# Kernel tuning notes

Hardware: AMD Instinct MI355X
Metric: run time of the kernel (lower is better)

Reference implementation:

```python
import jax, jax.numpy as jnp
import numpy as np

EPS = 1e-5
NH = 4          # num_heads
DH = 128        # head_dim
ALPHA = 1.0 / float(np.sqrt(DH))


def _ln(x, w, b):
    m = x.mean(-1, keepdims=True)
    v = x.var(-1, keepdims=True)
    return (x - m) * jax.lax.rsqrt(v + EPS) * w + b


def setup_inputs() -> dict:
    key = jax.random.key(0)
    ks = jax.random.split(key, 8)
    D = 512                 # hidden_size
    U = 4 * NH * DH         # uvqk linear out = 2048
    B, S, H = 32, 256, 2048  # batch, new tokens/seq, history len/seq
    NT = B * S              # 8192 flattened jagged tokens
    layer_input = jax.random.normal(ks[0], (NT, D), dtype=jnp.float32)
    hist_k = jax.random.normal(ks[1], (B, H, NH, DH), dtype=jnp.float32) * 0.1
    hist_v = jax.random.normal(ks[2], (B, H, NH, DH), dtype=jnp.float32) * 0.1
    # torch init: uniform(-0.5, 0.5); scaled down for numerical sanity
    W_uvqk = (jax.random.uniform(ks[3], (D, U), dtype=jnp.float32) - 0.5) * 0.1
    b_uvqk = (jax.random.uniform(ks[4], (U,), dtype=jnp.float32) - 0.5) * 0.1
    ln_in_w = jnp.ones((D,), jnp.float32)
    ln_in_b = jnp.zeros((D,), jnp.float32)
    ln_out_w = jnp.ones((NH * DH,), jnp.float32)
    ln_out_b = jnp.zeros((NH * DH,), jnp.float32)
    W_proj = jax.random.normal(ks[5], (NH * DH, D), dtype=jnp.float32) * 0.05
    return {
        "layer_input": layer_input, "hist_k": hist_k, "hist_v": hist_v,
        "ln_in_w": ln_in_w, "ln_in_b": ln_in_b,
        "W_uvqk": W_uvqk, "b_uvqk": b_uvqk,
        "ln_out_w": ln_out_w, "ln_out_b": ln_out_b, "W_proj": W_proj,
    }


def reference(layer_input, hist_k, hist_v, ln_in_w, ln_in_b,
              W_uvqk, b_uvqk, ln_out_w, ln_out_b, W_proj):
    B, H, nh, dh = hist_k.shape
    NT, D = layer_input.shape
    S = NT // B
    dspl = nh * dh
    # ln -> linear+bias -> silu (fused u,v,q,k projection)
    x = _ln(layer_input, ln_in_w, ln_in_b)
    uvqk = jax.nn.silu(x @ W_uvqk + b_uvqk)
    u, v, q, k = jnp.split(uvqk, 4, axis=-1)   # order: user, value, query, key
    q = q.reshape(B, S, nh, dh)
    k = k.reshape(B, S, nh, dh)
    v = v.reshape(B, S, nh, dh)
    # paged KV-cache append == concat new k,v after history
    K = jnp.concatenate([hist_k, k], axis=1)   # [B, T, nh, dh], T = H+S
    V = jnp.concatenate([hist_v, v], axis=1)
    T = H + S
    # HSTU varlen attention: silu(alpha * q k^T) with causal delta-q mask,
    # query i sits at global position H+i and may attend to kv pos <= H+i
    scores = jnp.einsum('bsnd,btnd->bnst', q, K) * ALPHA
    mask = jnp.arange(T)[None, :] <= (H + jnp.arange(S))[:, None]  # [S, T]
    p = jnp.where(mask[None, None], jax.nn.silu(scores), 0.0)
    attn = jnp.einsum('bnst,btnd->bsnd', p, V).reshape(NT, dspl)
    # gated output LN, projection, residual
    parallel = u * _ln(attn, ln_out_w, ln_out_b)
    return parallel @ W_proj + layer_input
```

## Files before the change

kernel.cpp:

```cpp
#include <hip/hip_runtime.h>
#include <hip/hip_bf16.h>


typedef __attribute__((ext_vector_type(8))) short v8s;
typedef __attribute__((ext_vector_type(4))) float v4f;
typedef __attribute__((ext_vector_type(4))) unsigned short v4us;
typedef __attribute__((ext_vector_type(4))) unsigned int v4u;

#define D_HID 512
#define U_DIM 2048
#define NHEAD 4
#define DHEAD 128
#define BATCH 32
#define SEQ   256
#define HIST  2048
#define NTOK  8192
#define ALPHA_ 0.08838834764831845f
#define EPS_   1e-5f

__device__ __forceinline__ unsigned short f2bf(float f) {
  unsigned int u = __float_as_uint(f);
  u += 0x7FFFu + ((u >> 16) & 1u);
  return (unsigned short)(u >> 16);
}
__device__ __forceinline__ float bf2f(unsigned short s) {
  return __uint_as_float(((unsigned int)s) << 16);
}
__device__ __forceinline__ float siluf(float x) {
  return x / (1.0f + __expf(-x));
}
__device__ __forceinline__ unsigned int cvtpk(float lo, float hi) {
  __hip_bfloat162 h = __float22bfloat162_rn(make_float2(lo, hi));
  union { __hip_bfloat162 h; unsigned int u; } cv; cv.h = h;
  return cv.u;
}

__global__ __launch_bounds__(256) void ln_in_kernel(
    const float* __restrict__ x, const float* __restrict__ w,
    const float* __restrict__ b, unsigned short* __restrict__ out)
{
  int wid = threadIdx.x >> 6, lane = threadIdx.x & 63;
  int row = blockIdx.x * 4 + wid;
  const float* xr = x + (size_t)row * D_HID + lane * 8;
  float4 a0 = *(const float4*)xr;
  float4 a1 = *(const float4*)(xr + 4);
  float v[8] = {a0.x, a0.y, a0.z, a0.w, a1.x, a1.y, a1.z, a1.w};
  float s = 0.f, s2 = 0.f;
#pragma unroll
  for (int j = 0; j < 8; ++j) { s += v[j]; s2 += v[j] * v[j]; }
#pragma unroll
  for (int m = 1; m < 64; m <<= 1) { s += __shfl_xor(s, m, 64); s2 += __shfl_xor(s2, m, 64); }
  float mean = s * (1.f / D_HID);
  float var  = s2 * (1.f / D_HID) - mean * mean;
  float rstd = rsqrtf(var + EPS_);
  const float* wp = w + lane * 8; const float* bp = b + lane * 8;
  float4 w0 = *(const float4*)wp, w1 = *(const float4*)(wp + 4);
  float4 b0 = *(const float4*)bp, b1 = *(const float4*)(bp + 4);
  float wv[8] = {w0.x, w0.y, w0.z, w0.w, w1.x, w1.y, w1.z, w1.w};
  float bv[8] = {b0.x, b0.y, b0.z, b0.w, b1.x, b1.y, b1.z, b1.w};
  v8s o;
#pragma unroll
  for (int j = 0; j < 8; ++j) o[j] = (short)f2bf((v[j] - mean) * rstd * wv[j] + bv[j]);
  *(v8s*)(out + (size_t)row * D_HID + lane * 8) = o;
}

__global__ __launch_bounds__(256) void gated_ln_kernel(
    const float* __restrict__ attn0, const float* __restrict__ attn1,
    const unsigned short* __restrict__ uvqk,
    const float* __restrict__ w, const float* __restrict__ b,
    unsigned short* __restrict__ par)
{
  int wid = threadIdx.x >> 6, lane = threadIdx.x & 63;
  int row = blockIdx.x * 4 + wid;
  size_t off = (size_t)row * D_HID + lane * 8;
  float4 x0 = *(const float4*)(attn0 + off), x1 = *(const float4*)(attn0 + off + 4);
  float4 y0 = *(const float4*)(attn1 + off), y1 = *(const float4*)(attn1 + off + 4);
  float v[8] = {x0.x + y0.x, x0.y + y0.y, x0.z + y0.z, x0.w + y0.w,
                x1.x + y1.x, x1.y + y1.y, x1.z + y1.z, x1.w + y1.w};
  float s = 0.f, s2 = 0.f;
#pragma unroll
  for (int j = 0; j < 8; ++j) { s += v[j]; s2 += v[j] * v[j]; }
#pragma unroll
  for (int m = 1; m < 64; m <<= 1) { s += __shfl_xor(s, m, 64); s2 += __shfl_xor(s2, m, 64); }
  float mean = s * (1.f / D_HID);
  float var  = s2 * (1.f / D_HID) - mean * mean;
  float rstd = rsqrtf(var + EPS_);
  const float* wp = w + lane * 8; const float* bp = b + lane * 8;
  float4 w0 = *(const float4*)wp, w1 = *(const float4*)(wp + 4);
  float4 b0 = *(const float4*)bp, b1 = *(const float4*)(bp + 4);
  float wv[8] = {w0.x, w0.y, w0.z, w0.w, w1.x, w1.y, w1.z, w1.w};
  float bv[8] = {b0.x, b0.y, b0.z, b0.w, b1.x, b1.y, b1.z, b1.w};
  v8s uv = *(const v8s*)(uvqk + (size_t)row * U_DIM + lane * 8);
  v8s o;
#pragma unroll
  for (int j = 0; j < 8; ++j) {
    float u = bf2f((unsigned short)uv[j]);
    o[j] = (short)f2bf(u * ((v[j] - mean) * rstd * wv[j] + bv[j]));
  }
  *(v8s*)(par + (size_t)row * D_HID + lane * 8) = o;
}

__global__ __launch_bounds__(256) void transpose_w_kernel(
    const float* __restrict__ in, unsigned short* __restrict__ out, int R, int C)
{
  __shared__ float tile[32][33];
  int c0 = blockIdx.x * 32, r0 = blockIdx.y * 32;
  int tr = threadIdx.x >> 3;
  int tc = (threadIdx.x & 7) * 4;
  float4 vv = *(const float4*)(in + (size_t)(r0 + tr) * C + c0 + tc);
  tile[tr][tc + 0] = vv.x; tile[tr][tc + 1] = vv.y;
  tile[tr][tc + 2] = vv.z; tile[tr][tc + 3] = vv.w;
  __syncthreads();
  v4us o;
#pragma unroll
  for (int j = 0; j < 4; ++j) o[j] = f2bf(tile[tc + j][tr]);
  *(v4us*)(out + (size_t)(c0 + tr) * R + r0 + tc) = o;
}

template <int EPI>
__global__ __launch_bounds__(256) void gemm_kernel(
    const unsigned short* __restrict__ A, const unsigned short* __restrict__ Bt,
    int K, int N,
    const float* __restrict__ bias, const float* __restrict__ resid,
    unsigned short* __restrict__ outb, float* __restrict__ outf)
{
  __shared__ unsigned short Al[128 * 40];
  __shared__ unsigned short Bl[128 * 40];
  int m0 = blockIdx.x * 128, n0 = blockIdx.y * 128;
  int tid = threadIdx.x, lane = tid & 63, wid = tid >> 6;
  int wr = wid >> 1, wc = wid & 1;
  int lr = lane & 15, lg = lane >> 4;

  v4f acc[4][4];
#pragma unroll
  for (int i = 0; i < 4; ++i)
#pragma unroll
    for (int j = 0; j < 4; ++j) acc[i][j] = (v4f){0.f, 0.f, 0.f, 0.f};

  int srow = tid >> 1;
  int sc   = (tid & 1) * 16;
  const unsigned short* ga = A  + (size_t)(m0 + srow) * K + sc;
  const unsigned short* gb = Bt + (size_t)(n0 + srow) * K + sc;

  for (int k0 = 0; k0 < K; k0 += 32) {
    v8s a0 = *(const v8s*)(ga + k0);
    v8s a1 = *(const v8s*)(ga + k0 + 8);
    v8s b0 = *(const v8s*)(gb + k0);
    v8s b1 = *(const v8s*)(gb + k0 + 8);
    *(v8s*)&Al[srow * 40 + sc]     = a0;
    *(v8s*)&Al[srow * 40 + sc + 8] = a1;
    *(v8s*)&Bl[srow * 40 + sc]     = b0;
    *(v8s*)&Bl[srow * 40 + sc + 8] = b1;
    __syncthreads();
    v8s af[4], bf[4];
#pragma unroll
    for (int mt = 0; mt < 4; ++mt) af[mt] = *(const v8s*)&Al[(wr * 64 + mt * 16 + lr) * 40 + lg * 8];
#pragma unroll
    for (int nt = 0; nt < 4; ++nt) bf[nt] = *(const v8s*)&Bl[(wc * 64 + nt * 16 + lr) * 40 + lg * 8];
#pragma unroll
    for (int mt = 0; mt < 4; ++mt)
#pragma unroll
      for (int nt = 0; nt < 4; ++nt)
        acc[mt][nt] = __builtin_amdgcn_mfma_f32_16x16x32_bf16(af[mt], bf[nt], acc[mt][nt], 0, 0, 0);
    __syncthreads();
  }

#pragma unroll
  for (int nt = 0; nt < 4; ++nt) {
    int col = n0 + wc * 64 + nt * 16 + lr;
    float bi = 0.f;
    if constexpr (EPI == 0) bi = bias[col];
#pragma unroll
    for (int mt = 0; mt < 4; ++mt) {
      int row0 = m0 + wr * 64 + mt * 16 + lg * 4;
#pragma unroll
      for (int r = 0; r < 4; ++r) {
        float xv = acc[mt][nt][r];
        if constexpr (EPI == 0) {
          float rv = siluf(xv + bi);
          if ((unsigned)(col - 2 * D_HID) < (unsigned)D_HID) rv *= ALPHA_;
          outb[(size_t)(row0 + r) * N + col] = f2bf(rv);
        } else {
          outf[(size_t)(row0 + r) * N + col] = xv + resid[(size_t)(row0 + r) * N + col];
        }
      }
    }
  }
}

__global__ __launch_bounds__(512) void attn_kernel(
    const float* __restrict__ histK, const float* __restrict__ histV,
    const unsigned short* __restrict__ uvqk, float* __restrict__ attn_out)
{
  __shared__ __align__(16) unsigned short Kl[2 * 64 * 136];
  __shared__ __align__(16) unsigned short Vt[2 * 128 * 72];
  __shared__ __align__(16) unsigned short Pl[8 * 32 * 72];

  int bid = blockIdx.x;
  int q   = bid >> 7;
  int b   = (bid >> 2) & 31;
  int n   = bid & 3;
  int tbase0 = q * 1152;
  const int NT = 18;

  int tid = threadIdx.x, lane = tid & 63, w = tid >> 6;
  int lr = lane & 15, lg = lane >> 4;

  v8s qf[2][4];
#pragma unroll
  for (int sb = 0; sb < 2; ++sb) {
    const unsigned short* qp = uvqk + (size_t)(b * SEQ + w * 32 + sb * 16 + lr) * U_DIM
                               + 2 * D_HID + n * DHEAD + lg * 8;
#pragma unroll
    for (int c = 0; c < 4; ++c) qf[sb][c] = *(const v8s*)(qp + c * 32);
  }

  v4f oacc[2][8];
#pragma unroll
  for (int sb = 0; sb < 2; ++sb)
#pragma unroll
    for (int dt = 0; dt < 8; ++dt) oacc[sb][dt] = (v4f){0.f, 0.f, 0.f, 0.f};

  int m     = tid & 15;
  int std0  = m * 8;
  int strow = tid >> 4;
  int vkey  = 8 * (m & 7);

  const float* kbase = histK + (((size_t)b * HIST) * NHEAD + n) * DHEAD + std0;
  const float* vbase = histV + (((size_t)b * HIST) * NHEAD + n) * DHEAD + std0;

  float4 hx[2][4];
  v8s    nx[2][2];
  int isnew_r = 0;

  auto stage_load = [&](int kt) {
    int tb = tbase0 + kt * 64;
    if (tb < HIST) {
      isnew_r = 0;
#pragma unroll
      for (int p = 0; p < 2; ++p) {
        size_t tg = (size_t)(tb + 2 * strow + p) * (NHEAD * DHEAD);
        hx[p][0] = *(const float4*)(kbase + tg);
        hx[p][1] = *(const float4*)(kbase + tg + 4);
        hx[p][2] = *(const float4*)(vbase + tg);
        hx[p][3] = *(const float4*)(vbase + tg + 4);
      }
    } else {
      isnew_r = 1;
#pragma unroll
      for (int p = 0; p < 2; ++p) {
        int srw = b * SEQ + (tb - HIST) + 2 * strow + p;
        nx[p][0] = *(const v8s*)(uvqk + (size_t)srw * U_DIM + 3 * D_HID + n * DHEAD + std0);
        nx[p][1] = *(const v8s*)(uvqk + (size_t)srw * U_DIM + 1 * D_HID + n * DHEAD + std0);
      }
    }
  };

  auto stage_store = [&](int buf) {
    unsigned short* Kb = &Kl[buf * (64 * 136)];
    unsigned short* Vb = &Vt[buf * (128 * 72)];
    int t0 = 2 * strow;
    if (!isnew_r) {
#pragma unroll
      for (int p = 0; p < 2; ++p) {
        v4u kp;
        kp[0] = cvtpk(hx[p][0].x, hx[p][0].y);
        kp[1] = cvtpk(hx[p][0].z, hx[p][0].w);
        kp[2] = cvtpk(hx[p][1].x, hx[p][1].y);
        kp[3] = cvtpk(hx[p][1].z, hx[p][1].w);
        *(v4u*)&Kb[(t0 + p) * 136 + std0] = kp;
      }
      float v0[8] = {hx[0][2].x, hx[0][2].y, hx[0][2].z, hx[0][2].w,
                     hx[0][3].x, hx[0][3].y, hx[0][3].z, hx[0][3].w};
      float v1[8] = {hx[1][2].x, hx[1][2].y, hx[1][2].z, hx[1][2].w,
                     hx[1][3].x, hx[1][3].y, hx[1][3].z, hx[1][3].w};
#pragma unroll
      for (int j = 0; j < 8; ++j) {
        int d = std0 + j;
        *(unsigned int*)&Vb[d * 72 + (t0 ^ vkey)] = cvtpk(v0[j], v1[j]);
      }
    } else {
#pragma unroll
      for (int p = 0; p < 2; ++p) *(v8s*)&Kb[(t0 + p) * 136 + std0] = nx[p][0];
#pragma unroll
      for (int j = 0; j < 8; ++j) {
        int d = std0 + j;
        unsigned int pk = (unsigned int)(unsigned short)nx[0][1][j]
                        | ((unsigned int)(unsigned short)nx[1][1][j] << 16);
        *(unsigned int*)&Vb[d * 72 + (t0 ^ vkey)] = pk;
      }
    }
  };

  stage_load(0);
  stage_store(0);
  stage_load(1);
  __syncthreads();

  unsigned short* Plw = &Pl[w * 32 * 72];

  for (int kt = 0; kt < NT; ++kt) {
    int cur = kt & 1;
    if (kt + 1 < NT) stage_store(cur ^ 1);
    if (kt + 2 < NT) stage_load(kt + 2);

    int tb = tbase0 + kt * 64;
    bool masked = (tb >= HIST);
    const unsigned short* Kb = &Kl[cur * (64 * 136)];
    const unsigned short* Vb = &Vt[cur * (128 * 72)];

    __builtin_amdgcn_s_setprio(1);
#pragma unroll
    for (int tt = 0; tt < 4; ++tt) {
      v8s kf[4];
#pragma unroll
      for (int c = 0; c < 4; ++c)
        kf[c] = *(const v8s*)&Kb[(tt * 16 + lr) * 136 + c * 32 + lg * 8];
#pragma unroll
      for (int sb = 0; sb < 2; ++sb) {
        v4f sa = (v4f){0.f, 0.f, 0.f, 0.f};
#pragma unroll
        for (int c = 0; c < 4; ++c)
          sa = __builtin_amdgcn_mfma_f32_16x16x32_bf16(kf[c], qf[sb][c], sa, 0, 0, 0);
        int s  = w * 32 + sb * 16 + lr;
        int t0 = tb + tt * 16 + lg * 4;
#pragma unroll
        for (int rp = 0; rp < 2; ++rp) {
          float p0 = siluf(sa[rp * 2]);
          float p1 = siluf(sa[rp * 2 + 1]);
          if (masked) {
            if (t0 + rp * 2     - HIST > s) p0 = 0.f;
            if (t0 + rp * 2 + 1 - HIST > s) p1 = 0.f;
          }
          *(unsigned int*)&Plw[(sb * 16 + lr) * 72 + tt * 16 + lg * 4 + rp * 2] =
              cvtpk(p0, p1);
        }
      }
    }

#pragma unroll
    for (int c = 0; c < 2; ++c) {
      v8s pa[2];
#pragma unroll
      for (int sb = 0; sb < 2; ++sb)
        pa[sb] = *(const v8s*)&Plw[(sb * 16 + lr) * 72 + c * 32 + lg * 8];
#pragma unroll
      for (int dt = 0; dt < 8; ++dt) {
        int d = dt * 16 + lr;
        int rkey = 8 * ((2 * dt + (lr >> 3)) & 7);
        v8s vf = *(const v8s*)&Vb[d * 72 + ((c * 32 + lg * 8) ^ rkey)];
#pragma unroll
        for (int sb = 0; sb < 2; ++sb)
          oacc[sb][dt] = __builtin_amdgcn_mfma_f32_16x16x32_bf16(pa[sb], vf, oacc[sb][dt], 0, 0, 0);
      }
    }
    __builtin_amdgcn_s_setprio(0);

    if (kt + 1 < NT) __syncthreads();
  }

#pragma unroll
  for (int sb = 0; sb < 2; ++sb) {
    int srow = b * SEQ + w * 32 + sb * 16 + lg * 4;
    float* op = attn_out + (size_t)q * ((size_t)NTOK * D_HID)
              + (size_t)srow * D_HID + n * DHEAD + lr;
#pragma unroll
    for (int dt = 0; dt < 8; ++dt)
#pragma unroll
      for (int r = 0; r < 4; ++r)
        op[(size_t)r * D_HID + dt * 16] = oacc[sb][dt][r];
  }
}

extern "C" void kernel_launch(void* const* d_in, const int* in_sizes, int n_in,
                              void* d_out, int out_size, void* d_ws, size_t ws_size,
                              hipStream_t stream)
{
  (void)in_sizes; (void)n_in; (void)out_size; (void)ws_size;

  const float* layer_input = (const float*)d_in[0];
  const float* hist_k   = (const float*)d_in[1];
  const float* hist_v   = (const float*)d_in[2];
  const float* ln_in_w  = (const float*)d_in[3];
  const float* ln_in_b  = (const float*)d_in[4];
  const float* W_uvqk   = (const float*)d_in[5];
  const float* b_uvqk   = (const float*)d_in[6];
  const float* ln_out_w = (const float*)d_in[7];
  const float* ln_out_b = (const float*)d_in[8];
  const float* W_proj   = (const float*)d_in[9];
  float* out = (float*)d_out;

  char* ws = (char*)d_ws;
  unsigned short* uvqk    = (unsigned short*)(ws);
  float*          attn0   = (float*)         (ws + (32u << 20));
  float*          attn1   = (float*)         (ws + (48u << 20));
  unsigned short* x_bf    = (unsigned short*)(ws + (48u << 20));
  unsigned short* par     = (unsigned short*)(ws + (64u << 20));
  unsigned short* wt_uvqk = (unsigned short*)(ws + (72u << 20));
  unsigned short* wt_proj = (unsigned short*)(ws + (74u << 20));

  ln_in_kernel<<<dim3(2048), dim3(256), 0, stream>>>(layer_input, ln_in_w, ln_in_b, x_bf);
  transpose_w_kernel<<<dim3(64, 16), dim3(256), 0, stream>>>(W_uvqk, wt_uvqk, 512, 2048);
  transpose_w_kernel<<<dim3(16, 16), dim3(256), 0, stream>>>(W_proj, wt_proj, 512, 512);
  gemm_kernel<0><<<dim3(64, 16), dim3(256), 0, stream>>>(x_bf, wt_uvqk, 512, 2048,
                                                         b_uvqk, nullptr, uvqk, nullptr);
  attn_kernel<<<dim3(256), dim3(512), 0, stream>>>(hist_k, hist_v, uvqk, attn0);
  gated_ln_kernel<<<dim3(2048), dim3(256), 0, stream>>>(attn0, attn1, uvqk, ln_out_w, ln_out_b, par);
  gemm_kernel<1><<<dim3(64, 4), dim3(256), 0, stream>>>(par, wt_proj, 512, 512,
                                                        nullptr, layer_input, nullptr, out);
}
```

Baseline: 189.2 us.

## Vectorize attention output stores via swapped MFMA operands, tweak silu and launch bounds

Swaps the A/B operands of the P·V MFMA so each lane holds four consecutive head-dim outputs, which lets the final attention output be written with float4 stores instead of scalar strided stores. Also uses a hardware reciprocal in silu, adds a min-blocks-per-CU hint of 2 to the attention kernel's launch bounds, and replaces 64-bit index math with 32-bit shifted offsets from precomputed base pointers in the tile loads. The occupancy hint may force register spills, and the approximate reciprocal slightly changes numerics.

```diff
diff --git a/kernel.cpp b/kernel.cpp
--- a/kernel.cpp
+++ b/kernel.cpp
@@ -27,7 +27,7 @@
   return __uint_as_float(((unsigned int)s) << 16);
 }
 __device__ __forceinline__ float siluf(float x) {
-  return x / (1.0f + __expf(-x));
+  return x * __builtin_amdgcn_rcpf(1.0f + __expf(-x));
 }
 __device__ __forceinline__ unsigned int cvtpk(float lo, float hi) {
   __hip_bfloat162 h = __float22bfloat162_rn(make_float2(lo, hi));
@@ -188,7 +188,7 @@
   }
 }
 
-__global__ __launch_bounds__(512) void attn_kernel(
+__global__ __launch_bounds__(512, 2) void attn_kernel(
     const float* __restrict__ histK, const float* __restrict__ histV,
     const unsigned short* __restrict__ uvqk, float* __restrict__ attn_out)
 {
@@ -228,6 +228,8 @@
 
   const float* kbase = histK + (((size_t)b * HIST) * NHEAD + n) * DHEAD + std0;
   const float* vbase = histV + (((size_t)b * HIST) * NHEAD + n) * DHEAD + std0;
+  const unsigned short* nkbase = uvqk + (size_t)(b * SEQ) * U_DIM + 3 * D_HID + n * DHEAD + std0;
+  const unsigned short* nvbase = uvqk + (size_t)(b * SEQ) * U_DIM + 1 * D_HID + n * DHEAD + std0;
 
   float4 hx[2][4];
   v8s    nx[2][2];
@@ -239,19 +241,19 @@
       isnew_r = 0;
 #pragma unroll
       for (int p = 0; p < 2; ++p) {
-        size_t tg = (size_t)(tb + 2 * strow + p) * (NHEAD * DHEAD);
-        hx[p][0] = *(const float4*)(kbase + tg);
-        hx[p][1] = *(const float4*)(kbase + tg + 4);
-        hx[p][2] = *(const float4*)(vbase + tg);
-        hx[p][3] = *(const float4*)(vbase + tg + 4);
+        unsigned off = ((unsigned)(tb + 2 * strow + p)) << 9;
+        hx[p][0] = *(const float4*)(kbase + off);
+        hx[p][1] = *(const float4*)(kbase + off + 4);
+        hx[p][2] = *(const float4*)(vbase + off);
+        hx[p][3] = *(const float4*)(vbase + off + 4);
       }
     } else {
       isnew_r = 1;
 #pragma unroll
       for (int p = 0; p < 2; ++p) {
-        int srw = b * SEQ + (tb - HIST) + 2 * strow + p;
-        nx[p][0] = *(const v8s*)(uvqk + (size_t)srw * U_DIM + 3 * D_HID + n * DHEAD + std0);
-        nx[p][1] = *(const v8s*)(uvqk + (size_t)srw * U_DIM + 1 * D_HID + n * DHEAD + std0);
+        unsigned off = ((unsigned)(tb - HIST + 2 * strow + p)) << 11;
+        nx[p][0] = *(const v8s*)(nkbase + off);
+        nx[p][1] = *(const v8s*)(nvbase + off);
       }
     }
   };
@@ -351,7 +353,7 @@
         v8s vf = *(const v8s*)&Vb[d * 72 + ((c * 32 + lg * 8) ^ rkey)];
 #pragma unroll
         for (int sb = 0; sb < 2; ++sb)
-          oacc[sb][dt] = __builtin_amdgcn_mfma_f32_16x16x32_bf16(pa[sb], vf, oacc[sb][dt], 0, 0, 0);
+          oacc[sb][dt] = __builtin_amdgcn_mfma_f32_16x16x32_bf16(vf, pa[sb], oacc[sb][dt], 0, 0, 0);
       }
     }
     __builtin_amdgcn_s_setprio(0);
@@ -361,14 +363,15 @@
 
 #pragma unroll
   for (int sb = 0; sb < 2; ++sb) {
-    int srow = b * SEQ + w * 32 + sb * 16 + lg * 4;
     float* op = attn_out + (size_t)q * ((size_t)NTOK * D_HID)
-              + (size_t)srow * D_HID + n * DHEAD + lr;
-#pragma unroll
-    for (int dt = 0; dt < 8; ++dt)
-#pragma unroll
-      for (int r = 0; r < 4; ++r)
-        op[(size_t)r * D_HID + dt * 16] = oacc[sb][dt][r];
+              + (size_t)(b * SEQ + w * 32 + sb * 16 + lr) * D_HID
+              + n * DHEAD + lg * 4;
+#pragma unroll
+    for (int dt = 0; dt < 8; ++dt) {
+      float4 o4 = make_float4(oacc[sb][dt][0], oacc[sb][dt][1],
+                              oacc[sb][dt][2], oacc[sb][dt][3]);
+      *(float4*)(op + dt * 16) = o4;
+    }
   }
 }
 
```

Result: faster. 173.2 us (-8.4%).
